# Kernel tuning notes

Measured on AMD Instinct MI355X. Metric: run time of the kernel, lower is better.

The kernel has to match this reference:

```python
import jax, jax.numpy as jnp
import numpy as np

MARGIN = 0.3
W_HUMAN = 1.0
W_PER = 1.0
NUM_CLASSES = 16
EPS = 1e-8


def setup_inputs() -> dict:
    key = jax.random.key(0)
    k1, k2, k3, k4, k5, k6 = jax.random.split(key, 6)
    B, D, T = 4096, 1024, 100000
    return {
        "preds_mat": jax.random.normal(k1, (B, NUM_CLASSES), dtype=jnp.float32),
        "preds_sub": jax.random.normal(k2, (B, 4), dtype=jnp.float32),
        "inputs": jax.random.normal(k3, (B, D), dtype=jnp.float32),
        "targets_mat": jax.random.randint(k4, (B,), 0, NUM_CLASSES, dtype=jnp.int64),
        "targets_sub": jax.random.randint(k5, (B,), 0, 4, dtype=jnp.int64),
        "user_answers": jax.random.randint(k6, (T, 3), 0, NUM_CLASSES, dtype=jnp.int64),
    }


def _pairwise_dist(x):
    # Euclidean pairwise distance: [B, B]
    sq = jnp.sum(x * x, axis=1)
    d2 = sq[:, None] + sq[None, :] - 2.0 * (x @ x.T)
    return jnp.sqrt(jnp.clip(d2, 1e-12))


def reference(preds_mat, preds_sub, inputs, targets_mat, targets_sub, user_answers):
    # Non-classification branch of TripletLossHuman.forward (is_classification=False, unit_norm=False).
    dist = _pairwise_dist(inputs)  # [B, B]

    # which of the NUM_CLASSES material labels are present in this batch
    present = jnp.zeros((NUM_CLASSES,), dtype=bool).at[targets_mat].set(True)
    # a human triplet (anchor,pos,neg labels) is usable iff all 3 labels are present
    valid = jnp.all(present[user_answers], axis=1)  # [T]

    # first occurrence index of each class label in targets_mat (matches torch nonzero()[0])
    first_idx = jnp.argmax(targets_mat[None, :] == jnp.arange(NUM_CLASSES)[:, None], axis=1)  # [C]

    ia = first_idx[user_answers[:, 0]]
    ip = first_idx[user_answers[:, 1]]
    ineg = first_idx[user_answers[:, 2]]
    dist_ap = dist[ia, ip]   # [T]
    dist_an = dist[ia, ineg]  # [T]

    n_valid = jnp.maximum(jnp.sum(valid.astype(dist.dtype)), 1.0)

    # MarginRankingLoss with y=-1: max(0, dist_ap - dist_an + margin), mean over valid triplets
    rank = jnp.maximum(dist_ap - dist_an + MARGIN, 0.0)
    loss_human = jnp.sum(jnp.where(valid, rank, 0.0)) / n_valid

    # perplexity loss
    s_ap = 1.0 / (dist_ap + 1.0)
    s_an = 1.0 / (dist_an + 1.0)
    p_ap = s_ap / (s_ap + s_an)
    per = -jnp.log(p_ap + EPS)
    loss_perplexity = jnp.sum(jnp.where(valid, per, 0.0)) / n_valid

    loss = W_HUMAN * loss_human + W_PER * loss_perplexity
    return jnp.stack([loss, loss_human, loss_perplexity])
```

## Files before the change

### kernel.cpp

```cpp
#include <hip/hip_runtime.h>
#include <math.h>

#define NUM_CLASSES 16
#define MARGIN_F 0.3f
#define EPS_F 1e-8f


__global__ __launch_bounds__(256) void k_first(const int* __restrict__ targets, int B,
                                               int* __restrict__ wsFirst,
                                               float* __restrict__ wsPresent,
                                               float* __restrict__ wsAcc) {
    __shared__ int fi[NUM_CLASSES];
    int t = threadIdx.x;
    if (t < NUM_CLASSES) fi[t] = 0x7fffffff;
    __syncthreads();
    for (int j = t; j < B; j += 256) {
        int c = targets[j];
        if (c >= 0 && c < NUM_CLASSES) atomicMin(&fi[c], j);
    }
    __syncthreads();
    if (t < NUM_CLASSES) {
        int v = fi[t];
        int pres = (v != 0x7fffffff);
        wsPresent[t] = pres ? 1.0f : 0.0f;
        wsFirst[t] = pres ? v : 0;
    }
    if (t < 3) wsAcc[t] = 0.0f;
}

__global__ __launch_bounds__(64) void k_dist(const float* __restrict__ x, int Dm,
                                             const int* __restrict__ wsFirst,
                                             float* __restrict__ D16) {
    int pair = blockIdx.x;
    int c1 = pair >> 4, c2 = pair & 15;
    const float* __restrict__ x1 = x + (long)wsFirst[c1] * Dm;
    const float* __restrict__ x2 = x + (long)wsFirst[c2] * Dm;
    int l = threadIdx.x;
    float dot = 0.f, s1 = 0.f, s2 = 0.f;
    for (int k = l; k < Dm; k += 64) {
        float a = x1[k], b = x2[k];
        dot = fmaf(a, b, dot);
        s1  = fmaf(a, a, s1);
        s2  = fmaf(b, b, s2);
    }
    #pragma unroll
    for (int off = 32; off > 0; off >>= 1) {
        dot += __shfl_down(dot, off);
        s1  += __shfl_down(s1, off);
        s2  += __shfl_down(s2, off);
    }
    if (l == 0) {
        float d2 = s1 + s2 - 2.0f * dot;
        D16[pair] = sqrtf(fmaxf(d2, 1e-12f));
    }
}

__global__ __launch_bounds__(256) void k_reduce(const int* __restrict__ ua, int T,
                                                const float* __restrict__ D16,
                                                const float* __restrict__ wsPresent,
                                                float* __restrict__ wsAcc) {
    __shared__ float sD[256];
    __shared__ float sP[NUM_CLASSES];
    __shared__ float sRed[4][3];
    int t = threadIdx.x;
    sD[t] = D16[t];
    if (t < NUM_CLASSES) sP[t] = wsPresent[t];
    __syncthreads();

    float r = 0.f, pp = 0.f, cnt = 0.f;
    for (int i = blockIdx.x * blockDim.x + t; i < T; i += gridDim.x * blockDim.x) {
        int a = ua[3 * i + 0];
        int b = ua[3 * i + 1];
        int c = ua[3 * i + 2];
        float valid = sP[a] * sP[b] * sP[c];
        float dap = sD[(a << 4) | b];
        float dan = sD[(a << 4) | c];
        float rank = fmaxf(dap - dan + MARGIN_F, 0.0f);
        float sap = 1.0f / (dap + 1.0f);
        float san = 1.0f / (dan + 1.0f);
        float per = -logf(sap / (sap + san) + EPS_F);
        r   += valid * rank;
        pp  += valid * per;
        cnt += valid;
    }
    #pragma unroll
    for (int off = 32; off > 0; off >>= 1) {
        r   += __shfl_down(r, off);
        pp  += __shfl_down(pp, off);
        cnt += __shfl_down(cnt, off);
    }
    int wave = t >> 6, lane = t & 63;
    if (lane == 0) { sRed[wave][0] = r; sRed[wave][1] = pp; sRed[wave][2] = cnt; }
    __syncthreads();
    if (t == 0) {
        float R = 0.f, P = 0.f, C = 0.f;
        #pragma unroll
        for (int w = 0; w < 4; ++w) { R += sRed[w][0]; P += sRed[w][1]; C += sRed[w][2]; }
        atomicAdd(&wsAcc[0], R);
        atomicAdd(&wsAcc[1], P);
        atomicAdd(&wsAcc[2], C);
    }
}

__global__ void k_final(const float* __restrict__ wsAcc, float* __restrict__ out) {
    float nv = fmaxf(wsAcc[2], 1.0f);
    float lh = wsAcc[0] / nv;
    float lp = wsAcc[1] / nv;
    out[0] = lh + lp;
    out[1] = lh;
    out[2] = lp;
}

extern "C" void kernel_launch(void* const* d_in, const int* in_sizes, int n_in,
                              void* d_out, int out_size, void* d_ws, size_t ws_size,
                              hipStream_t stream) {
    const float* x       = (const float*)d_in[2];
    const int*   targets = (const int*)d_in[3];
    const int*   ua      = (const int*)d_in[5];
    float* out = (float*)d_out;

    int B  = in_sizes[3];
    int Dm = in_sizes[2] / B;
    int T  = in_sizes[5] / 3;

    float* ws      = (float*)d_ws;
    float* D16     = ws;
    int*   wsFirst = (int*)(ws + 256);
    float* wsPres  = ws + 272;
    float* wsAcc   = ws + 288;

    k_first<<<1, 256, 0, stream>>>(targets, B, wsFirst, wsPres, wsAcc);
    k_dist<<<256, 64, 0, stream>>>(x, Dm, wsFirst, D16);
    k_reduce<<<512, 256, 0, stream>>>(ua, T, D16, wsPres, wsAcc);
    k_final<<<1, 1, 0, stream>>>(wsAcc, out);
}
```

Measured before the change: 106.7 us.

## Fuse first-index and distance kernels, fold finalize into reduce via last-block counter

The first-occurrence search and the 16x16 distance computation now run in one 1024-thread block: squared norms are computed once per class and reused, and each wave computes 16 dot products. The finalize step moves into the reduce kernel through a threadfence plus atomic completion counter, so the last block writes the output. The reduce grid is also halved to 256 blocks. Together these cut the launch count from four to two, but the distance work now runs on a single CU instead of 256 blocks.

```diff
diff --git a/kernel.cpp b/kernel.cpp
--- a/kernel.cpp
+++ b/kernel.cpp
@@ -6,15 +6,18 @@
 #define EPS_F 1e-8f
 
 
-__global__ __launch_bounds__(256) void k_first(const int* __restrict__ targets, int B,
-                                               int* __restrict__ wsFirst,
-                                               float* __restrict__ wsPresent,
-                                               float* __restrict__ wsAcc) {
-    __shared__ int fi[NUM_CLASSES];
+__global__ __launch_bounds__(1024) void kA(const float* __restrict__ x, int Dm,
+                                           const int* __restrict__ targets, int B,
+                                           float* __restrict__ D16,
+                                           float* __restrict__ wsPres,
+                                           float* __restrict__ wsAcc,
+                                           int* __restrict__ wsCnt) {
+    __shared__ int   fi[NUM_CLASSES];
+    __shared__ float sSq[NUM_CLASSES];
     int t = threadIdx.x;
     if (t < NUM_CLASSES) fi[t] = 0x7fffffff;
     __syncthreads();
-    for (int j = t; j < B; j += 256) {
+    for (int j = t; j < B; j += 1024) {
         int c = targets[j];
         if (c >= 0 && c < NUM_CLASSES) atomicMin(&fi[c], j);
     }
@@ -22,49 +25,53 @@
     if (t < NUM_CLASSES) {
         int v = fi[t];
         int pres = (v != 0x7fffffff);
-        wsPresent[t] = pres ? 1.0f : 0.0f;
-        wsFirst[t] = pres ? v : 0;
+        wsPres[t] = pres ? 1.0f : 0.0f;
+        fi[t] = pres ? v : 0;
     }
     if (t < 3) wsAcc[t] = 0.0f;
-}
+    if (t == 3) *wsCnt = 0;
+    __syncthreads();
 
-__global__ __launch_bounds__(64) void k_dist(const float* __restrict__ x, int Dm,
-                                             const int* __restrict__ wsFirst,
-                                             float* __restrict__ D16) {
-    int pair = blockIdx.x;
-    int c1 = pair >> 4, c2 = pair & 15;
-    const float* __restrict__ x1 = x + (long)wsFirst[c1] * Dm;
-    const float* __restrict__ x2 = x + (long)wsFirst[c2] * Dm;
-    int l = threadIdx.x;
-    float dot = 0.f, s1 = 0.f, s2 = 0.f;
-    for (int k = l; k < Dm; k += 64) {
-        float a = x1[k], b = x2[k];
-        dot = fmaf(a, b, dot);
-        s1  = fmaf(a, a, s1);
-        s2  = fmaf(b, b, s2);
+    int wave = t >> 6, lane = t & 63;
+
+    {
+        const float* __restrict__ row = x + (long)fi[wave] * Dm;
+        float s = 0.f;
+        for (int k = lane; k < Dm; k += 64) { float a = row[k]; s = fmaf(a, a, s); }
+        #pragma unroll
+        for (int off = 32; off > 0; off >>= 1) s += __shfl_down(s, off);
+        if (lane == 0) sSq[wave] = s;
     }
-    #pragma unroll
-    for (int off = 32; off > 0; off >>= 1) {
-        dot += __shfl_down(dot, off);
-        s1  += __shfl_down(s1, off);
-        s2  += __shfl_down(s2, off);
-    }
-    if (l == 0) {
-        float d2 = s1 + s2 - 2.0f * dot;
-        D16[pair] = sqrtf(fmaxf(d2, 1e-12f));
+    __syncthreads();
+
+    for (int pair = wave; pair < 256; pair += 16) {
+        int c1 = pair >> 4, c2 = pair & 15;
+        const float* __restrict__ x1 = x + (long)fi[c1] * Dm;
+        const float* __restrict__ x2 = x + (long)fi[c2] * Dm;
+        float dot = 0.f;
+        for (int k = lane; k < Dm; k += 64) dot = fmaf(x1[k], x2[k], dot);
+        #pragma unroll
+        for (int off = 32; off > 0; off >>= 1) dot += __shfl_down(dot, off);
+        if (lane == 0) {
+            float d2 = sSq[c1] + sSq[c2] - 2.0f * dot;
+            D16[pair] = sqrtf(fmaxf(d2, 1e-12f));
+        }
     }
 }
 
-__global__ __launch_bounds__(256) void k_reduce(const int* __restrict__ ua, int T,
-                                                const float* __restrict__ D16,
-                                                const float* __restrict__ wsPresent,
-                                                float* __restrict__ wsAcc) {
+__global__ __launch_bounds__(256) void kB(const int* __restrict__ ua, int T,
+                                          const float* __restrict__ D16,
+                                          const float* __restrict__ wsPres,
+                                          float* __restrict__ wsAcc,
+                                          int* __restrict__ wsCnt,
+                                          float* __restrict__ out) {
     __shared__ float sD[256];
     __shared__ float sP[NUM_CLASSES];
     __shared__ float sRed[4][3];
+    __shared__ bool  amLast;
     int t = threadIdx.x;
     sD[t] = D16[t];
-    if (t < NUM_CLASSES) sP[t] = wsPresent[t];
+    if (t < NUM_CLASSES) sP[t] = wsPres[t];
     __syncthreads();
 
     float r = 0.f, pp = 0.f, cnt = 0.f;
@@ -99,16 +106,22 @@
         atomicAdd(&wsAcc[0], R);
         atomicAdd(&wsAcc[1], P);
         atomicAdd(&wsAcc[2], C);
+        __threadfence();
+        int done = atomicAdd(wsCnt, 1);
+        amLast = (done == (int)gridDim.x - 1);
     }
-}
-
-__global__ void k_final(const float* __restrict__ wsAcc, float* __restrict__ out) {
-    float nv = fmaxf(wsAcc[2], 1.0f);
-    float lh = wsAcc[0] / nv;
-    float lp = wsAcc[1] / nv;
-    out[0] = lh + lp;
-    out[1] = lh;
-    out[2] = lp;
+    __syncthreads();
+    if (amLast && t == 0) {
+        float R  = atomicAdd(&wsAcc[0], 0.0f);
+        float P  = atomicAdd(&wsAcc[1], 0.0f);
+        float C  = atomicAdd(&wsAcc[2], 0.0f);
+        float nv = fmaxf(C, 1.0f);
+        float lh = R / nv;
+        float lp = P / nv;
+        out[0] = lh + lp;
+        out[1] = lh;
+        out[2] = lp;
+    }
 }
 
 extern "C" void kernel_launch(void* const* d_in, const int* in_sizes, int n_in,
@@ -123,14 +136,12 @@
     int Dm = in_sizes[2] / B;
     int T  = in_sizes[5] / 3;
 
-    float* ws      = (float*)d_ws;
-    float* D16     = ws;
-    int*   wsFirst = (int*)(ws + 256);
-    float* wsPres  = ws + 272;
-    float* wsAcc   = ws + 288;
+    float* ws     = (float*)d_ws;
+    float* D16    = ws;
+    float* wsPres = ws + 256;
+    float* wsAcc  = ws + 272;
+    int*   wsCnt  = (int*)(ws + 275);
 
-    k_first<<<1, 256, 0, stream>>>(targets, B, wsFirst, wsPres, wsAcc);
-    k_dist<<<256, 64, 0, stream>>>(x, Dm, wsFirst, D16);
-    k_reduce<<<512, 256, 0, stream>>>(ua, T, D16, wsPres, wsAcc);
-    k_final<<<1, 1, 0, stream>>>(wsAcc, out);
+    kA<<<1, 1024, 0, stream>>>(x, Dm, targets, B, D16, wsPres, wsAcc, wsCnt);
+    kB<<<256, 256, 0, stream>>>(ua, T, D16, wsPres, wsAcc, wsCnt, out);
 }
```

New measurement: 127.2 us. 19.2% more time.
